# Performance work log

Measured on AMD Instinct MI355X. Metric: run time of the kernel, lower is better.

Reference implementation:

```python
import math
import jax, jax.numpy as jnp
import numpy as np

B, N, C, HEADS, EXTRA = 16, 577, 768, 12, 1
IMG = (24, 24)
LAMBDA = 0.6


def make_rel_index():
    Hh, Ww = IMG
    coords = np.stack(np.meshgrid(np.arange(Hh), np.arange(Ww), indexing='ij')).reshape(2, -1)
    rel = (coords[:, :, None] - coords[:, None, :]).transpose(1, 2, 0).astype(np.int64)
    rel[..., 0] += Hh - 1
    rel[..., 1] += Ww - 1
    rel[..., 0] *= 2 * Ww - 1
    idx = rel.sum(-1)
    idx = np.pad(idx, ((EXTRA, 0), (EXTRA, 0)))  # pad extra-token rows/cols with index 0
    return jnp.asarray(idx, dtype=jnp.int32)


def setup_inputs() -> dict:
    key = jax.random.key(0)
    ks = jax.random.split(key, 4)
    x = jax.random.normal(ks[0], (B, N, C), jnp.float32)
    qkv_w = jax.random.normal(ks[1], (3 * C, C), jnp.float32) * 0.02
    proj_w = jax.random.normal(ks[2], (C, C), jnp.float32) * 0.02
    proj_b = jnp.zeros((C,), jnp.float32)
    table_sz = (2 * IMG[0] - 1) * (2 * IMG[1] - 1) + 1  # 2210
    bias_table = jax.random.normal(ks[3], (table_sz, HEADS), jnp.float32) * 0.02
    token_weights = jnp.array([0.5, 0.5], jnp.float32)  # softmax([.5,.5]) at init
    return {"x": x, "qkv_w": qkv_w, "proj_w": proj_w, "proj_b": proj_b,
            "bias_table": bias_table, "token_weights": token_weights,
            "rel_index": make_rel_index()}


def attention(x, qkv_w, proj_w, proj_b, bias_table, rel_index):
    b, n, c = x.shape
    hd = c // HEADS
    scale = hd ** -0.5
    qkv = (x @ qkv_w.T).reshape(b, n, 3, HEADS, hd).transpose(2, 0, 3, 1, 4)
    q, k, v = qkv[0] * scale, qkv[1], qkv[2]  # (b,H,n,hd)
    attn = jnp.einsum('bhnd,bhmd->bhnm', q, k)
    bias = jnp.transpose(bias_table[rel_index], (2, 0, 1))  # (H,N,N)
    attn = jax.nn.softmax(attn + bias[None], axis=-1)
    out = jnp.einsum('bhnm,bhmd->bhnd', attn, v).transpose(0, 2, 1, 3).reshape(b, n, c)
    return out @ proj_w.T + proj_b, attn


def select_indices(attn, token_weights):
    # eager, data-dependent sizing (mirrors torch .tolist()/set() host logic)
    n = N - EXTRA
    cls_attn = attn[:, :, 0, EXTRA:].mean(axis=1)  # (B, n)
    avg = cls_attn.mean(axis=1, keepdims=True)
    mx = cls_attn.max(axis=1, keepdims=True)
    counts = np.asarray(((cls_attn >= avg) & (cls_attn <= mx)).sum(axis=1))
    T = counts.sum() / counts.shape[0]
    sig = 1.0 / (1.0 + math.exp(-(float(counts.max()) - float(T)) / B))
    keep = int(round(n * (LAMBDA + (1.0 - LAMBDA) * sig)))
    avg_extra = attn[:, :, :EXTRA, EXTRA:].mean(axis=1)  # (B, EXTRA, n)
    all_idx = []
    for e in range(EXTRA):
        ti = jax.lax.top_k(avg_extra[:, e, :], keep)[1]
        all_idx.extend(np.asarray(ti).reshape(-1).tolist())
    keep_idx = np.array(list(dict.fromkeys(all_idx))[:keep], dtype=np.int32)
    remaining = N - (EXTRA + keep)
    w = jax.nn.softmax(token_weights)
    num_text = int(float(w[0]) * remaining)
    num_img = remaining - num_text
    kt, ki = jax.random.split(jax.random.key(1))
    text_idx = jax.random.randint(kt, (B, max(num_text, 0)), 0, EXTRA)
    img_idx = jax.random.randint(ki, (B, max(num_img, 0)), 0, n - EXTRA)
    return jnp.asarray(keep_idx), text_idx, img_idx


def assemble(x_out, y, keep_idx, text_idx, img_idx):
    b, _, c = x_out.shape
    x_sel = x_out[:, EXTRA:][:, keep_idx]  # shared indices across batch
    parts = [x_out[:, :EXTRA], x_sel]
    if text_idx.shape[1] > 0:
        text_tokens = y[:, 1:1 + EXTRA]
        gi = jnp.broadcast_to(text_idx[:, :, None], (b, text_idx.shape[1], c))
        parts.append(jnp.take_along_axis(text_tokens, gi, axis=1))
    if img_idx.shape[1] > 0:
        image_tokens = y[:, 1 + EXTRA:]
        gi = jnp.broadcast_to(img_idx[:, :, None], (b, img_idx.shape[1], c))
        parts.append(jnp.take_along_axis(image_tokens, gi, axis=1))
    return jnp.concatenate(parts, axis=1)


def reference(x, qkv_w, proj_w, proj_b, bias_table, token_weights, rel_index):
    out, attn = attention(x, qkv_w, proj_w, proj_b, bias_table, rel_index)
    keep_idx, text_idx, img_idx = select_indices(attn, token_weights)
    return assemble(out, x, keep_idx, text_idx, img_idx)
```

## Files before the change

### kernel.cpp

```cpp
#include <hip/hip_runtime.h>
#include <math.h>

#define B_    16
#define N_    577
#define C_    768
#define H_    12
#define HD_   64
#define M_    (B_ * N_)
#define QKV_N 2304
#define QK32_N 1536
#define NIMG  576
#define BIAS_DIM 640

typedef _Float16 half8  __attribute__((ext_vector_type(8)));
typedef _Float16 half4v __attribute__((ext_vector_type(4)));
typedef float    floatx4 __attribute__((ext_vector_type(4)));

#define OFF_QKV32    0u
#define OFF_ATTNH    0u
#define OFF_ATTNL    3545088u
#define OFF_XOUT     7090176u
#define OFF_QKVH     14180352u
#define OFF_QKVL     24815616u
#define OFF_CLS      35450880u
#define OFF_CLSPART  35460096u
#define OFF_META     35570688u
#define OFF_WQKVH    35582976u
#define OFF_WQKVL    36467712u
#define OFF_WPROJH   37352448u
#define OFF_WPROJL   37647360u
#define OFF_BIASPAD  37942272u

__global__ __launch_bounds__(256) void split_kernel(const float* __restrict__ in,
                                                    _Float16* __restrict__ hi,
                                                    _Float16* __restrict__ lo, int n) {
    int i = (blockIdx.x * 256 + threadIdx.x) * 4;
    if (i >= n) return;
    float4 v = *(const float4*)(in + i);
    half4v h, l;
    float vv[4] = {v.x, v.y, v.z, v.w};
#pragma unroll
    for (int j = 0; j < 4; ++j) {
        _Float16 hj = (_Float16)vv[j];
        h[j] = hj;
        l[j] = (_Float16)(vv[j] - (float)hj);
    }
    *(half4v*)(hi + i) = h;
    *(half4v*)(lo + i) = l;
}

__global__ __launch_bounds__(256) void bias_expand(const float* __restrict__ bias_table,
                                                   const int* __restrict__ rel_index,
                                                   _Float16* __restrict__ bias_pad) {
    int i = blockIdx.x, h = blockIdx.y;
    _Float16* dst = bias_pad + ((size_t)h * BIAS_DIM + i) * BIAS_DIM;
    const _Float16 NEG = (_Float16)(-30000.f);
    if (i < N_) {
        const int* ri = rel_index + (size_t)i * N_;
        for (int j = threadIdx.x; j < BIAS_DIM; j += 256)
            dst[j] = (j < N_) ? (_Float16)bias_table[ri[j] * H_ + h] : NEG;
    } else {
        for (int j = threadIdx.x; j < BIAS_DIM; j += 256) dst[j] = NEG;
    }
}

__global__ __launch_bounds__(256) void hgemm_qkv(const float* __restrict__ A,
                                                 const _Float16* __restrict__ Bh,
                                                 const _Float16* __restrict__ Bl,
                                                 float* __restrict__ qkv32,
                                                 _Float16* __restrict__ qh_,
                                                 _Float16* __restrict__ ql_) {
    const int K = 768;
    __shared__ __attribute__((aligned(16))) _Float16 Ah_s[128][40];
    __shared__ __attribute__((aligned(16))) _Float16 Al_s[128][40];
    __shared__ __attribute__((aligned(16))) _Float16 Bh_s[128][40];
    __shared__ __attribute__((aligned(16))) _Float16 Bl_s[128][40];

    int tid = threadIdx.x;
    int wave = tid >> 6, lane = tid & 63;
    int g = lane >> 4, c = lane & 15;
    int wr = wave >> 1, wc = wave & 1;
    int m0 = blockIdx.y * 128, n0 = blockIdx.x * 128;

    floatx4 acc[4][4];
#pragma unroll
    for (int mi = 0; mi < 4; ++mi)
#pragma unroll
        for (int ni = 0; ni < 4; ++ni) { acc[mi][ni][0] = 0.f; acc[mi][ni][1] = 0.f; acc[mi][ni][2] = 0.f; acc[mi][ni][3] = 0.f; }

    int lr = tid >> 2;
    int lc = (tid & 3) << 3;

    for (int k0 = 0; k0 < K; k0 += 32) {
        __syncthreads();
#pragma unroll
        for (int hh = 0; hh < 2; ++hh) {
            int r2 = lr + hh * 64;
            int arow = m0 + r2; if (arow >= M_) arow = M_ - 1;
            const float* ap = A + (size_t)arow * K + k0 + lc;
            floatx4 a0 = *(const floatx4*)ap;
            floatx4 a1 = *(const floatx4*)(ap + 4);
            half8 ah, al;
#pragma unroll
            for (int i = 0; i < 4; ++i) {
                _Float16 h0 = (_Float16)a0[i];
                ah[i] = h0; al[i] = (_Float16)(a0[i] - (float)h0);
                _Float16 h1 = (_Float16)a1[i];
                ah[i + 4] = h1; al[i + 4] = (_Float16)(a1[i] - (float)h1);
            }
            *(half8*)&Ah_s[r2][lc] = ah;
            *(half8*)&Al_s[r2][lc] = al;
            size_t gb = (size_t)(n0 + r2) * K + k0 + lc;
            *(half8*)&Bh_s[r2][lc] = *(const half8*)(Bh + gb);
            *(half8*)&Bl_s[r2][lc] = *(const half8*)(Bl + gb);
        }
        __syncthreads();

        half8 af_h[4], af_l[4];
#pragma unroll
        for (int mi = 0; mi < 4; ++mi) {
            af_h[mi] = *(const half8*)&Ah_s[wr * 64 + mi * 16 + c][g * 8];
            af_l[mi] = *(const half8*)&Al_s[wr * 64 + mi * 16 + c][g * 8];
        }
#pragma unroll
        for (int ni = 0; ni < 4; ++ni) {
            half8 bf_h = *(const half8*)&Bh_s[wc * 64 + ni * 16 + c][g * 8];
            half8 bf_l = *(const half8*)&Bl_s[wc * 64 + ni * 16 + c][g * 8];
#pragma unroll
            for (int mi = 0; mi < 4; ++mi) {
                acc[mi][ni] = __builtin_amdgcn_mfma_f32_16x16x32_f16(af_h[mi], bf_h, acc[mi][ni], 0, 0, 0);
                acc[mi][ni] = __builtin_amdgcn_mfma_f32_16x16x32_f16(af_h[mi], bf_l, acc[mi][ni], 0, 0, 0);
                acc[mi][ni] = __builtin_amdgcn_mfma_f32_16x16x32_f16(af_l[mi], bf_h, acc[mi][ni], 0, 0, 0);
            }
        }
    }

#pragma unroll
    for (int ni = 0; ni < 4; ++ni) {
        int col = n0 + wc * 64 + ni * 16 + c;
#pragma unroll
        for (int mi = 0; mi < 4; ++mi) {
#pragma unroll
            for (int r = 0; r < 4; ++r) {
                int row = m0 + wr * 64 + mi * 16 + 4 * g + r;
                if (row < M_) {
                    float v = acc[mi][ni][r];
                    if (col < QK32_N) qkv32[(size_t)row * QK32_N + col] = v;
                    float sv = (col < 768) ? v * 0.125f : v;
                    _Float16 hi = (_Float16)sv;
                    size_t idx = (size_t)row * QKV_N + col;
                    qh_[idx] = hi;
                    ql_[idx] = (_Float16)(sv - (float)hi);
                }
            }
        }
    }
}

__global__ __launch_bounds__(256) void hgemm_nt_split(const _Float16* __restrict__ Ah,
                                                      const _Float16* __restrict__ Al,
                                                      const _Float16* __restrict__ Bh,
                                                      const _Float16* __restrict__ Bl,
                                                      const float* __restrict__ bias,
                                                      float* __restrict__ Cout,
                                                      int M, int Nout) {
    const int K = 768;
    __shared__ __attribute__((aligned(16))) _Float16 Ah_s[128][40];
    __shared__ __attribute__((aligned(16))) _Float16 Al_s[128][40];
    __shared__ __attribute__((aligned(16))) _Float16 Bh_s[128][40];
    __shared__ __attribute__((aligned(16))) _Float16 Bl_s[128][40];

    int tid = threadIdx.x;
    int wave = tid >> 6, lane = tid & 63;
    int g = lane >> 4, c = lane & 15;
    int wr = wave >> 1, wc = wave & 1;
    int m0 = blockIdx.y * 128, n0 = blockIdx.x * 128;

    floatx4 acc[4][4];
#pragma unroll
    for (int mi = 0; mi < 4; ++mi)
#pragma unroll
        for (int ni = 0; ni < 4; ++ni) { acc[mi][ni][0] = 0.f; acc[mi][ni][1] = 0.f; acc[mi][ni][2] = 0.f; acc[mi][ni][3] = 0.f; }

    int lr = tid >> 2;
    int lc = (tid & 3) << 3;

    for (int k0 = 0; k0 < K; k0 += 32) {
        __syncthreads();
#pragma unroll
        for (int hh = 0; hh < 2; ++hh) {
            int r2 = lr + hh * 64;
            size_t ga = (size_t)(m0 + r2) * K + k0 + lc;
            size_t gb = (size_t)(n0 + r2) * K + k0 + lc;
            *(half8*)&Ah_s[r2][lc] = *(const half8*)(Ah + ga);
            *(half8*)&Al_s[r2][lc] = *(const half8*)(Al + ga);
            *(half8*)&Bh_s[r2][lc] = *(const half8*)(Bh + gb);
            *(half8*)&Bl_s[r2][lc] = *(const half8*)(Bl + gb);
        }
        __syncthreads();

        half8 af_h[4], af_l[4];
#pragma unroll
        for (int mi = 0; mi < 4; ++mi) {
            af_h[mi] = *(const half8*)&Ah_s[wr * 64 + mi * 16 + c][g * 8];
            af_l[mi] = *(const half8*)&Al_s[wr * 64 + mi * 16 + c][g * 8];
        }
#pragma unroll
        for (int ni = 0; ni < 4; ++ni) {
            half8 bf_h = *(const half8*)&Bh_s[wc * 64 + ni * 16 + c][g * 8];
            half8 bf_l = *(const half8*)&Bl_s[wc * 64 + ni * 16 + c][g * 8];
#pragma unroll
            for (int mi = 0; mi < 4; ++mi) {
                acc[mi][ni] = __builtin_amdgcn_mfma_f32_16x16x32_f16(af_h[mi], bf_h, acc[mi][ni], 0, 0, 0);
                acc[mi][ni] = __builtin_amdgcn_mfma_f32_16x16x32_f16(af_h[mi], bf_l, acc[mi][ni], 0, 0, 0);
                acc[mi][ni] = __builtin_amdgcn_mfma_f32_16x16x32_f16(af_l[mi], bf_h, acc[mi][ni], 0, 0, 0);
            }
        }
    }

#pragma unroll
    for (int ni = 0; ni < 4; ++ni) {
        int col = n0 + wc * 64 + ni * 16 + c;
        float bv = bias ? bias[col] : 0.f;
#pragma unroll
        for (int mi = 0; mi < 4; ++mi) {
#pragma unroll
            for (int r = 0; r < 4; ++r) {
                int row = m0 + wr * 64 + mi * 16 + 4 * g + r;
                if (row < M) Cout[(size_t)row * Nout + col] = acc[mi][ni][r] + bv;
            }
        }
    }
}

__global__ __launch_bounds__(256, 3) void attn_mfma(const _Float16* __restrict__ qkvh,
                                                    const _Float16* __restrict__ qkvl,
                                                    const _Float16* __restrict__ bias_pad,
                                                    _Float16* __restrict__ attnh,
                                                    _Float16* __restrict__ attnl) {
    __shared__ __attribute__((aligned(16))) _Float16 Kh[64][72];
    __shared__ __attribute__((aligned(16))) _Float16 Kl[64][72];
    __shared__ __attribute__((aligned(16))) _Float16 VhS[64 * 64];
    __shared__ __attribute__((aligned(16))) _Float16 VlS[64 * 64];
    __shared__ __attribute__((aligned(16))) _Float16 Pb[4][32][72];

    int bh = blockIdx.y;
    int h = bh >> 4, b = bh & 15;
    int tid = threadIdx.x;
    int wave = tid >> 6, lane = tid & 63;
    int g = lane >> 4, c = lane & 15;
    int row0 = blockIdx.x * 128 + wave * 32;
    char* vhb = (char*)VhS;
    char* vlb = (char*)VlS;

    half8 qh[2][2], ql[2][2];
#pragma unroll
    for (int rt = 0; rt < 2; ++rt) {
        int grow = row0 + rt * 16 + c;
#pragma unroll
        for (int kb = 0; kb < 2; ++kb) {
            half8 zh = {}, zl = {};
            if (grow < N_) {
                size_t off = (size_t)(b * N_ + grow) * QKV_N + h * HD_ + kb * 32 + g * 8;
                zh = *(const half8*)(qkvh + off);
                zl = *(const half8*)(qkvl + off);
            }
            qh[rt][kb] = zh; ql[rt][kb] = zl;
        }
    }

    floatx4 o[2][4];
    float mrun[2][4], lrun[2][4];
#pragma unroll
    for (int rt = 0; rt < 2; ++rt) {
#pragma unroll
        for (int t = 0; t < 4; ++t) { o[rt][t][0] = 0.f; o[rt][t][1] = 0.f; o[rt][t][2] = 0.f; o[rt][t][3] = 0.f; }
#pragma unroll
        for (int r = 0; r < 4; ++r) { mrun[rt][r] = -1e30f; lrun[rt][r] = 0.f; }
    }

    for (int j0 = 0; j0 < N_; j0 += 64) {
        __syncthreads();
#pragma unroll
        for (int pass = 0; pass < 2; ++pass) {
            int idx = pass * 256 + tid;
            int key = idx >> 3;
            int d0 = (idx & 7) << 3;
            int j = j0 + key;
            half8 khv = {}, klv = {}, vhv = {}, vlv = {};
            if (j < N_) {
                size_t gb = (size_t)(b * N_ + j) * QKV_N + h * HD_ + d0;
                khv = *(const half8*)(qkvh + gb + 768);
                klv = *(const half8*)(qkvl + gb + 768);
                vhv = *(const half8*)(qkvh + gb + 1536);
                vlv = *(const half8*)(qkvl + gb + 1536);
            }
            *(half8*)&Kh[key][d0] = khv;
            *(half8*)&Kl[key][d0] = klv;
#pragma unroll
            for (int i = 0; i < 8; ++i) {
                int d = d0 + i;
                int cb = (key * 2) ^ (((d & 7) ^ ((d >> 3) & 7)) << 4);
                *(_Float16*)(vhb + d * 128 + cb) = vhv[i];
                *(_Float16*)(vlb + d * 128 + cb) = vlv[i];
            }
        }
        __syncthreads();

        float bv[2][4][4];
#pragma unroll
        for (int rt = 0; rt < 2; ++rt)
#pragma unroll
            for (int t = 0; t < 4; ++t)
#pragma unroll
                for (int r = 0; r < 4; ++r)
                    bv[rt][t][r] = (float)bias_pad[((size_t)h * BIAS_DIM + row0 + rt * 16 + 4 * g + r) * BIAS_DIM
                                                   + j0 + t * 16 + c];

        floatx4 s[2][4];
#pragma unroll
        for (int rt = 0; rt < 2; ++rt)
#pragma unroll
            for (int t = 0; t < 4; ++t) { s[rt][t][0] = 0.f; s[rt][t][1] = 0.f; s[rt][t][2] = 0.f; s[rt][t][3] = 0.f; }
#pragma unroll
        for (int t = 0; t < 4; ++t) {
#pragma unroll
            for (int kb = 0; kb < 2; ++kb) {
                half8 kh8 = *(const half8*)&Kh[t * 16 + c][kb * 32 + g * 8];
                half8 kl8 = *(const half8*)&Kl[t * 16 + c][kb * 32 + g * 8];
#pragma unroll
                for (int rt = 0; rt < 2; ++rt) {
                    s[rt][t] = __builtin_amdgcn_mfma_f32_16x16x32_f16(qh[rt][kb], kh8, s[rt][t], 0, 0, 0);
                    s[rt][t] = __builtin_amdgcn_mfma_f32_16x16x32_f16(qh[rt][kb], kl8, s[rt][t], 0, 0, 0);
                    s[rt][t] = __builtin_amdgcn_mfma_f32_16x16x32_f16(ql[rt][kb], kh8, s[rt][t], 0, 0, 0);
                }
            }
        }

#pragma unroll
        for (int rt = 0; rt < 2; ++rt) {
#pragma unroll
            for (int t = 0; t < 4; ++t)
#pragma unroll
                for (int r = 0; r < 4; ++r) s[rt][t][r] += bv[rt][t][r];
            float pm[4], mnew[4], corr[4], rs[4];
#pragma unroll
            for (int r = 0; r < 4; ++r)
                pm[r] = fmaxf(fmaxf(s[rt][0][r], s[rt][1][r]), fmaxf(s[rt][2][r], s[rt][3][r]));
#pragma unroll
            for (int r = 0; r < 4; ++r) {
                pm[r] = fmaxf(pm[r], __shfl_xor(pm[r], 1));
                pm[r] = fmaxf(pm[r], __shfl_xor(pm[r], 2));
                pm[r] = fmaxf(pm[r], __shfl_xor(pm[r], 4));
                pm[r] = fmaxf(pm[r], __shfl_xor(pm[r], 8));
                mnew[r] = fmaxf(mrun[rt][r], pm[r]);
                corr[r] = __expf(mrun[rt][r] - mnew[r]);
                rs[r] = 0.f;
            }
#pragma unroll
            for (int t = 0; t < 4; ++t)
#pragma unroll
                for (int r = 0; r < 4; ++r) {
                    float p = __expf(s[rt][t][r] - mnew[r]);
                    s[rt][t][r] = p;
                    rs[r] += p;
                }
#pragma unroll
            for (int r = 0; r < 4; ++r) {
                rs[r] += __shfl_xor(rs[r], 1);
                rs[r] += __shfl_xor(rs[r], 2);
                rs[r] += __shfl_xor(rs[r], 4);
                rs[r] += __shfl_xor(rs[r], 8);
                lrun[rt][r] = lrun[rt][r] * corr[r] + rs[r];
                mrun[rt][r] = mnew[r];
            }
#pragma unroll
            for (int t = 0; t < 4; ++t)
#pragma unroll
                for (int r = 0; r < 4; ++r) o[rt][t][r] *= corr[r];
#pragma unroll
            for (int t = 0; t < 4; ++t)
#pragma unroll
                for (int r = 0; r < 4; ++r)
                    Pb[wave][rt * 16 + 4 * g + r][t * 16 + c] = (_Float16)s[rt][t][r];
        }

#pragma unroll
        for (int kb = 0; kb < 2; ++kb) {
            half8 pa[2];
#pragma unroll
            for (int rt = 0; rt < 2; ++rt)
                pa[rt] = *(const half8*)&Pb[wave][rt * 16 + c][kb * 32 + g * 8];
#pragma unroll
            for (int t = 0; t < 4; ++t) {
                int row = t * 16 + c;
                int cb = (kb * 64 + g * 16) ^ (((row & 7) ^ ((row >> 3) & 7)) << 4);
                half8 vh8 = *(const half8*)(vhb + row * 128 + cb);
                half8 vl8 = *(const half8*)(vlb + row * 128 + cb);
#pragma unroll
                for (int rt = 0; rt < 2; ++rt) {
                    o[rt][t] = __builtin_amdgcn_mfma_f32_16x16x32_f16(pa[rt], vh8, o[rt][t], 0, 0, 0);
                    o[rt][t] = __builtin_amdgcn_mfma_f32_16x16x32_f16(pa[rt], vl8, o[rt][t], 0, 0, 0);
                }
            }
        }
    }

#pragma unroll
    for (int rt = 0; rt < 2; ++rt)
#pragma unroll
        for (int t = 0; t < 4; ++t)
#pragma unroll
            for (int r = 0; r < 4; ++r) {
                int row = row0 + rt * 16 + 4 * g + r;
                if (row < N_) {
                    float val = o[rt][t][r] / lrun[rt][r];
                    size_t idx = (size_t)(b * N_ + row) * C_ + h * HD_ + t * 16 + c;
                    _Float16 hi = (_Float16)val;
                    attnh[idx] = hi;
                    attnl[idx] = (_Float16)(val - (float)hi);
                }
            }
}

__global__ __launch_bounds__(256) void cls_head_kernel(const float* __restrict__ qkv32,
                                                       const float* __restrict__ bias_table,
                                                       const int* __restrict__ rel_index,
                                                       float* __restrict__ cls_part) {
    int b = blockIdx.x, h = blockIdx.y;
    __shared__ float q0[64];
    __shared__ float s[N_];
    __shared__ float red[256];
    int tid = threadIdx.x;
    if (tid < 64) q0[tid] = qkv32[(size_t)(b * N_) * QK32_N + h * HD_ + tid] * 0.125f;
    __syncthreads();
    for (int j = tid; j < N_; j += 256) {
        const float* kr = qkv32 + (size_t)(b * N_ + j) * QK32_N + 768 + h * HD_;
        float d = 0.f;
        for (int kk = 0; kk < 64; ++kk) d += q0[kk] * kr[kk];
        s[j] = d + bias_table[rel_index[j] * H_ + h];
    }
    __syncthreads();
    float mx = -1e30f;
    for (int j = tid; j < N_; j += 256) mx = fmaxf(mx, s[j]);
    red[tid] = mx;
    __syncthreads();
    for (int st = 128; st > 0; st >>= 1) {
        if (tid < st) red[tid] = fmaxf(red[tid], red[tid + st]);
        __syncthreads();
    }
    float m = red[0];
    __syncthreads();
    float ssum = 0.f;
    for (int j = tid; j < N_; j += 256) ssum += expf(s[j] - m);
    red[tid] = ssum;
    __syncthreads();
    for (int st = 128; st > 0; st >>= 1) {
        if (tid < st) red[tid] += red[tid + st];
        __syncthreads();
    }
    float tot = red[0];
    __syncthreads();
    float* dst = cls_part + (size_t)(b * H_ + h) * NIMG;
    for (int j = tid; j < NIMG; j += 256) dst[j] = expf(s[j + 1] - m) / tot;
}

__global__ __launch_bounds__(576) void cls_reduce_kernel(const float* __restrict__ cls_part,
                                                         float* __restrict__ cls) {
    int b = blockIdx.x;
    int j = threadIdx.x;
    float a = 0.f;
    for (int h = 0; h < H_; ++h) a += cls_part[(size_t)(b * H_ + h) * NIMG + j];
    cls[b * NIMG + j] = a * (1.0f / 12.0f);
}

__device__ __forceinline__ void tf2x32(unsigned k0, unsigned k1, unsigned x0, unsigned x1,
                                       unsigned& o0, unsigned& o1) {
    unsigned ks2 = k0 ^ k1 ^ 0x1BD11BDAu;
    x0 += k0; x1 += k1;
#define ROTL_(v, d) (((v) << (d)) | ((v) >> (32 - (d))))
#define RND_(d) { x0 += x1; x1 = ROTL_(x1, d); x1 ^= x0; }
    RND_(13) RND_(15) RND_(26) RND_(6)
    x0 += k1; x1 += ks2 + 1u;
    RND_(17) RND_(29) RND_(16) RND_(24)
    x0 += ks2; x1 += k0 + 2u;
    RND_(13) RND_(15) RND_(26) RND_(6)
    x0 += k0; x1 += k1 + 3u;
    RND_(17) RND_(29) RND_(16) RND_(24)
    x0 += k1; x1 += ks2 + 4u;
    RND_(13) RND_(15) RND_(26) RND_(6)
    x0 += ks2; x1 += k0 + 5u;
    o0 = x0; o1 = x1;
#undef RND_
#undef ROTL_
}

__global__ __launch_bounds__(256) void select_kernel(const float* __restrict__ cls,
                                                     const float* __restrict__ token_w,
                                                     int* __restrict__ meta,
                                                     int* __restrict__ keep_idx,
                                                     int* __restrict__ img_idx) {
    __shared__ float red[256];
    __shared__ int ired[256];
    __shared__ int counts[16];
    __shared__ float c0[NIMG];
    __shared__ int keep_sh, nimg_sh;
    int tid = threadIdx.x;

    for (int b = 0; b < 16; ++b) {
        float sm = 0.f;
        for (int j = tid; j < NIMG; j += 256) sm += cls[b * NIMG + j];
        red[tid] = sm;
        __syncthreads();
        for (int st = 128; st > 0; st >>= 1) {
            if (tid < st) red[tid] += red[tid + st];
            __syncthreads();
        }
        float avg = red[0] * (1.0f / 576.0f);
        __syncthreads();
        int cnt = 0;
        for (int j = tid; j < NIMG; j += 256) cnt += (cls[b * NIMG + j] >= avg) ? 1 : 0;
        ired[tid] = cnt;
        __syncthreads();
        for (int st = 128; st > 0; st >>= 1) {
            if (tid < st) ired[tid] += ired[tid + st];
            __syncthreads();
        }
        if (tid == 0) counts[b] = ired[0];
        __syncthreads();
    }

    if (tid == 0) {
        int csum = 0, cmax = 0;
        for (int b2 = 0; b2 < 16; ++b2) {
            csum += counts[b2];
            if (counts[b2] > cmax) cmax = counts[b2];
        }
        double T = (double)csum / 16.0;
        double sig = 1.0 / (1.0 + exp(-(((double)cmax) - T) / 16.0));
        double kd = 576.0 * (0.6 + 0.4 * sig);
        int keep = (int)llrint(kd);
        int remaining = NIMG - keep;
        float w0 = token_w[0], w1 = token_w[1];
        float wm = fmaxf(w0, w1);
        float e0 = expf(w0 - wm), e1 = expf(w1 - wm);
        float wsm = e0 / (e0 + e1);
        int ntext = (int)((double)wsm * (double)remaining);
        int nimg = remaining - ntext;
        meta[0] = keep; meta[1] = ntext; meta[2] = nimg;
        keep_sh = keep; nimg_sh = nimg;
    }
    __syncthreads();

    for (int j = tid; j < NIMG; j += 256) c0[j] = cls[j];
    __syncthreads();
    int keep = keep_sh;
    for (int j = tid; j < NIMG; j += 256) {
        float v = c0[j];
        int rank = 0;
        for (int j2 = 0; j2 < NIMG; ++j2) {
            float v2 = c0[j2];
            rank += ((v2 > v) || (v2 == v && j2 < j)) ? 1 : 0;
        }
        if (rank < keep) keep_idx[rank] = j;
    }

    unsigned ki0, ki1, k1a, k1b, k2a, k2b;
    tf2x32(0u, 1u, 0u, 1u, ki0, ki1);
    tf2x32(ki0, ki1, 0u, 0u, k1a, k1b);
    tf2x32(ki0, ki1, 0u, 1u, k2a, k2b);
    int nimg = nimg_sh;
    int S = 16 * nimg;
    const unsigned span = 575u;
    const unsigned mult = ((65536u % span) * (65536u % span)) % span;
    for (int i = tid; i < S; i += 256) {
        unsigned h0, h1, l0, l1;
        tf2x32(k1a, k1b, 0u, (unsigned)i, h0, h1);
        tf2x32(k2a, k2b, 0u, (unsigned)i, l0, l1);
        unsigned hb = h0 ^ h1;
        unsigned lb = l0 ^ l1;
        unsigned off = ((hb % span) * mult + (lb % span)) % span;
        img_idx[i] = (int)off;
    }
}

__global__ __launch_bounds__(192) void assemble_kernel(const float* __restrict__ xout,
                                                       const float* __restrict__ x,
                                                       const int* __restrict__ meta,
                                                       const int* __restrict__ keep_idx,
                                                       const int* __restrict__ img_idx,
                                                       float* __restrict__ out) {
    int gb = blockIdx.x;
    int token = gb % N_;
    int b = gb / N_;
    int keep = meta[0], ntext = meta[1], nimg = meta[2];
    const float* src;
    if (token == 0) {
        src = xout + (size_t)(b * N_) * C_;
    } else if (token <= keep) {
        src = xout + (size_t)(b * N_ + 1 + keep_idx[token - 1]) * C_;
    } else if (token <= keep + ntext) {
        src = x + (size_t)(b * N_ + 1) * C_;
    } else {
        int t = token - 1 - keep - ntext;
        src = x + (size_t)(b * N_ + 2 + img_idx[b * nimg + t]) * C_;
    }
    float4* d = (float4*)(out + (size_t)(b * N_ + token) * C_);
    d[threadIdx.x] = ((const float4*)src)[threadIdx.x];
}

extern "C" void kernel_launch(void* const* d_in, const int* in_sizes, int n_in,
                              void* d_out, int out_size, void* d_ws, size_t ws_size,
                              hipStream_t stream) {
    const float* x          = (const float*)d_in[0];
    const float* qkv_w      = (const float*)d_in[1];
    const float* proj_w     = (const float*)d_in[2];
    const float* proj_b     = (const float*)d_in[3];
    const float* bias_table = (const float*)d_in[4];
    const float* token_w    = (const float*)d_in[5];
    const int*   rel_index  = (const int*)d_in[6];
    float* out = (float*)d_out;
    float* ws  = (float*)d_ws;

    float*     qkv32    = ws + OFF_QKV32;
    _Float16*  attnh    = (_Float16*)(ws + OFF_ATTNH);
    _Float16*  attnl    = (_Float16*)(ws + OFF_ATTNL);
    float*     xout     = ws + OFF_XOUT;
    _Float16*  qkvh     = (_Float16*)(ws + OFF_QKVH);
    _Float16*  qkvl     = (_Float16*)(ws + OFF_QKVL);
    float*     cls      = ws + OFF_CLS;
    float*     cls_part = ws + OFF_CLSPART;
    int*       meta     = (int*)(ws + OFF_META);
    int*       keep_idx = meta + 8;
    int*       img_idx  = keep_idx + 576;
    _Float16*  wqkvh    = (_Float16*)(ws + OFF_WQKVH);
    _Float16*  wqkvl    = (_Float16*)(ws + OFF_WQKVL);
    _Float16*  wprojh   = (_Float16*)(ws + OFF_WPROJH);
    _Float16*  wprojl   = (_Float16*)(ws + OFF_WPROJL);
    _Float16*  bias_pad = (_Float16*)(ws + OFF_BIASPAD);

    split_kernel<<<dim3(QKV_N * C_ / 1024), 256, 0, stream>>>(qkv_w, wqkvh, wqkvl, QKV_N * C_);
    split_kernel<<<dim3(C_ * C_ / 1024), 256, 0, stream>>>(proj_w, wprojh, wprojl, C_ * C_);
    bias_expand<<<dim3(BIAS_DIM, H_), 256, 0, stream>>>(bias_table, rel_index, bias_pad);
    hgemm_qkv<<<dim3(QKV_N / 128, (M_ + 127) / 128), 256, 0, stream>>>(
        x, wqkvh, wqkvl, qkv32, qkvh, qkvl);
    cls_head_kernel<<<dim3(B_, H_), 256, 0, stream>>>(qkv32, bias_table, rel_index, cls_part);
    cls_reduce_kernel<<<dim3(B_), 576, 0, stream>>>(cls_part, cls);
    select_kernel<<<dim3(1), 256, 0, stream>>>(cls, token_w, meta, keep_idx, img_idx);
    attn_mfma<<<dim3((N_ + 127) / 128, B_ * H_), 256, 0, stream>>>(
        qkvh, qkvl, bias_pad, attnh, attnl);
    hgemm_nt_split<<<dim3(C_ / 128, (M_ + 127) / 128), 256, 0, stream>>>(
        attnh, attnl, wprojh, wprojl, proj_b, xout, M_, C_);
    assemble_kernel<<<dim3(B_ * N_), 192, 0, stream>>>(
        xout, x, meta, keep_idx, img_idx, out);
}
```

Before: 633.4 us.

## Prefetch next K/V tile into registers and remap attention grid for XCD locality

The attention kernel now loads the next 64-key K/V tile from global memory into registers while the current tile is being computed, then writes it to shared memory at the start of the following iteration. This hides global load latency behind the MFMA work. The launch grid is also flattened, and block IDs are remapped so that all row blocks of one (batch, head) land on the same XCD, which should improve L2 reuse of K/V. The cost is extra registers for the prefetch buffers, which could reduce occupancy under the 3-blocks launch bound.

Result: slower. 658.2 us (+3.9%).

```diff
diff --git a/kernel.cpp b/kernel.cpp
--- a/kernel.cpp
+++ b/kernel.cpp
@@ -11,6 +11,7 @@
 #define QK32_N 1536
 #define NIMG  576
 #define BIAS_DIM 640
+#define ROWBLK 5
 
 typedef _Float16 half8  __attribute__((ext_vector_type(8)));
 typedef _Float16 half4v __attribute__((ext_vector_type(4)));
@@ -244,12 +245,17 @@
     __shared__ __attribute__((aligned(16))) _Float16 VlS[64 * 64];
     __shared__ __attribute__((aligned(16))) _Float16 Pb[4][32][72];
 
-    int bh = blockIdx.y;
-    int h = bh >> 4, b = bh & 15;
+    int id = blockIdx.x;
+    int xcd = id & 7;
+    int slot = id >> 3;
+    int gg = slot / ROWBLK;
+    int rblk = slot - gg * ROWBLK;
+    int grp = gg * 8 + xcd;
+    int h = grp >> 4, b = grp & 15;
     int tid = threadIdx.x;
     int wave = tid >> 6, lane = tid & 63;
     int g = lane >> 4, c = lane & 15;
-    int row0 = blockIdx.x * 128 + wave * 32;
+    int row0 = rblk * 128 + wave * 32;
     char* vhb = (char*)VhS;
     char* vlb = (char*)VlS;
 
@@ -279,33 +285,47 @@
         for (int r = 0; r < 4; ++r) { mrun[rt][r] = -1e30f; lrun[rt][r] = 0.f; }
     }
 
+    int skey = tid >> 3;
+    int sd0 = (tid & 7) << 3;
+    half8 nk_h[2], nk_l[2], nv_h[2], nv_l[2];
+
+    auto load_tile = [&](int j0) {
+#pragma unroll
+        for (int p = 0; p < 2; ++p) {
+            int j = j0 + p * 32 + skey;
+            half8 a = {}, bb = {}, cc = {}, dd = {};
+            if (j < N_) {
+                size_t gb = (size_t)(b * N_ + j) * QKV_N + h * HD_ + sd0;
+                a  = *(const half8*)(qkvh + gb + 768);
+                bb = *(const half8*)(qkvl + gb + 768);
+                cc = *(const half8*)(qkvh + gb + 1536);
+                dd = *(const half8*)(qkvl + gb + 1536);
+            }
+            nk_h[p] = a; nk_l[p] = bb; nv_h[p] = cc; nv_l[p] = dd;
+        }
+    };
+    auto store_tile = [&]() {
+#pragma unroll
+        for (int p = 0; p < 2; ++p) {
+            int key = p * 32 + skey;
+            *(half8*)&Kh[key][sd0] = nk_h[p];
+            *(half8*)&Kl[key][sd0] = nk_l[p];
+#pragma unroll
+            for (int i = 0; i < 8; ++i) {
+                int d = sd0 + i;
+                int cb = (key * 2) ^ (((d & 7) ^ ((d >> 3) & 7)) << 4);
+                *(_Float16*)(vhb + d * 128 + cb) = nv_h[p][i];
+                *(_Float16*)(vlb + d * 128 + cb) = nv_l[p][i];
+            }
+        }
+    };
+
+    load_tile(0);
     for (int j0 = 0; j0 < N_; j0 += 64) {
         __syncthreads();
-#pragma unroll
-        for (int pass = 0; pass < 2; ++pass) {
-            int idx = pass * 256 + tid;
-            int key = idx >> 3;
-            int d0 = (idx & 7) << 3;
-            int j = j0 + key;
-            half8 khv = {}, klv = {}, vhv = {}, vlv = {};
-            if (j < N_) {
-                size_t gb = (size_t)(b * N_ + j) * QKV_N + h * HD_ + d0;
-                khv = *(const half8*)(qkvh + gb + 768);
-                klv = *(const half8*)(qkvl + gb + 768);
-                vhv = *(const half8*)(qkvh + gb + 1536);
-                vlv = *(const half8*)(qkvl + gb + 1536);
-            }
-            *(half8*)&Kh[key][d0] = khv;
-            *(half8*)&Kl[key][d0] = klv;
-#pragma unroll
-            for (int i = 0; i < 8; ++i) {
-                int d = d0 + i;
-                int cb = (key * 2) ^ (((d & 7) ^ ((d >> 3) & 7)) << 4);
-                *(_Float16*)(vhb + d * 128 + cb) = vhv[i];
-                *(_Float16*)(vlb + d * 128 + cb) = vlv[i];
-            }
-        }
-        __syncthreads();
+        store_tile();
+        __syncthreads();
+        if (j0 + 64 < N_) load_tile(j0 + 64);
 
         float bv[2][4][4];
 #pragma unroll
@@ -647,7 +667,7 @@
     cls_head_kernel<<<dim3(B_, H_), 256, 0, stream>>>(qkv32, bias_table, rel_index, cls_part);
     cls_reduce_kernel<<<dim3(B_), 576, 0, stream>>>(cls_part, cls);
     select_kernel<<<dim3(1), 256, 0, stream>>>(cls, token_w, meta, keep_idx, img_idx);
-    attn_mfma<<<dim3((N_ + 127) / 128, B_ * H_), 256, 0, stream>>>(
+    attn_mfma<<<dim3(ROWBLK * B_ * H_), 256, 0, stream>>>(
         qkvh, qkvl, bias_pad, attnh, attnl);
     hgemm_nt_split<<<dim3(C_ / 128, (M_ + 127) / 128), 256, 0, stream>>>(
         attnh, attnl, wprojh, wprojl, proj_b, xout, M_, C_);
```
